# Kernel tuning notes

Hardware: AMD Instinct MI355X
Metric: run time of the kernel (lower is better)

The kernel has to match this reference:

```python
import jax, jax.numpy as jnp
from jax import lax
import numpy as np

B, CIN, COUT, S = 2, 64, 128, 12
H1, H2 = CIN * 4, COUT * 4          # MBConv hidden dims (expand_ratio=4)
HEADS = 8
MLP_HID = COUT * 4                   # transformer mlp_ratio=4
EPS = 1e-5


def conv1x1(x, w, b=None):
    # 1x1x1 Conv3d == channel matmul. w: [out, in], x: [B,C,H,W,D]
    y = jnp.einsum('oc,bchwd->bohwd', w, x)
    if b is not None:
        y = y + b[None, :, None, None, None]
    return y


def inorm(x, g, b):
    # InstanceNorm3d(affine=True): per-sample, per-channel over spatial dims
    m = x.mean(axis=(2, 3, 4), keepdims=True)
    v = x.var(axis=(2, 3, 4), keepdims=True)
    return (x - m) * jax.lax.rsqrt(v + EPS) * g[None, :, None, None, None] + b[None, :, None, None, None]


def gnorm(x, g, b, groups):
    Bb, C, H, W, D = x.shape
    xr = x.reshape(Bb, groups, C // groups, H, W, D)
    m = xr.mean(axis=(2, 3, 4, 5), keepdims=True)
    v = xr.var(axis=(2, 3, 4, 5), keepdims=True)
    xr = (xr - m) * jax.lax.rsqrt(v + EPS)
    return xr.reshape(Bb, C, H, W, D) * g[None, :, None, None, None] + b[None, :, None, None, None]


def dwconv3(x, w):
    # depthwise 3x3x3, stride 1, pad 1. w: [C,1,3,3,3]
    return lax.conv_general_dilated(
        x, w, window_strides=(1, 1, 1), padding=[(1, 1)] * 3,
        dimension_numbers=('NCDHW', 'OIDHW', 'NCDHW'),
        feature_group_count=x.shape[1])


def mbconv(x, ew, g1, b1, dw, g2, b2, sw1, sb1, sw2, sb2, pw, g3, b3, use_residual):
    res = x
    h = jax.nn.silu(inorm(conv1x1(x, ew), g1, b1))        # expand 1x1
    h = jax.nn.silu(inorm(dwconv3(h, dw), g2, b2))        # depthwise 3x3x3
    s = h.mean(axis=(2, 3, 4), keepdims=True)             # SE: squeeze
    s = jax.nn.silu(conv1x1(s, sw1, sb1))
    s = jax.nn.sigmoid(conv1x1(s, sw2, sb2))
    h = h * s
    h = inorm(conv1x1(h, pw), g3, b3)                     # project
    return res + h if use_residual else h


def mhsa(x, qkv_w, proj_w, proj_b):
    Bb, C, H, W, D = x.shape
    N = H * W * D
    hd = C // HEADS
    qkv = conv1x1(x, qkv_w).reshape(Bb, 3, HEADS, hd, N)
    qkv = jnp.transpose(qkv, (1, 0, 2, 4, 3))             # [3,B,h,N,hd]
    q, k, v = qkv[0], qkv[1], qkv[2]
    attn = jax.nn.softmax(jnp.einsum('bhnd,bhmd->bhnm', q, k) * (hd ** -0.5), axis=-1)
    out = jnp.einsum('bhnm,bhmd->bhnd', attn, v)          # [B,h,N,hd]
    out = jnp.transpose(out, (0, 1, 3, 2)).reshape(Bb, C, H, W, D)
    return conv1x1(out, proj_w, proj_b)


def transformer_block(x, n1g, n1b, qkv, pw, pb, n2g, n2b, mw1, mb1, mw2, mb2):
    x = x + mhsa(gnorm(x, n1g, n1b, min(32, x.shape[1])), qkv, pw, pb)
    h = gnorm(x, n2g, n2b, min(32, x.shape[1]))
    h = conv1x1(jax.nn.gelu(conv1x1(h, mw1, mb1), approximate=False), mw2, mb2)
    return x + h


def shuffle_attn(x, cw1, cw2, gng, gnb, sw):
    b, c, h, w, d = x.shape
    G = 4
    gc = c // (2 * G)  # group_channels
    x6 = x.reshape(b, G, 2 * gc, h, w, d)
    x0 = x6[:, :, :gc].reshape(b * G, gc, h, w, d)
    x1 = x6[:, :, gc:].reshape(b * G, gc, h, w, d)
    # channel branch
    a = x0.mean(axis=(2, 3, 4), keepdims=True)
    a = conv1x1(jax.nn.silu(conv1x1(a, cw1)), cw2)
    x0 = jax.nn.sigmoid(a) * x0
    # spatial branch: GroupNorm(max(1,gc//8)=2 groups) + 1x1 conv
    sgn = gnorm(x1, gng, gnb, max(1, gc // 8))
    x1 = jax.nn.sigmoid(conv1x1(sgn, sw)) * x1
    out = jnp.concatenate([x0.reshape(b, G * gc, h, w, d), x1.reshape(b, G * gc, h, w, d)], axis=1)
    # channel shuffle
    out = out.reshape(b, G, 2 * gc, h, w, d).transpose(0, 2, 1, 3, 4, 5).reshape(b, c, h, w, d)
    return out


def setup_inputs() -> dict:
    key = jax.random.key(0)
    ks = iter(jax.random.split(key, 64))
    w = lambda *shape: jax.random.normal(next(ks), shape, jnp.float32) * 0.05
    p = {}
    p['x'] = jax.random.normal(next(ks), (B, CIN, S, S, S), jnp.float32)
    # mbconv1 (in=64 -> hidden=256 -> out=128), SE reduced = 256//4 = 64
    r1 = H1 // 4
    p['m1_ew'] = w(H1, CIN); p['m1_g1'] = jnp.ones(H1); p['m1_b1'] = jnp.zeros(H1)
    p['m1_dw'] = w(H1, 1, 3, 3, 3); p['m1_g2'] = jnp.ones(H1); p['m1_b2'] = jnp.zeros(H1)
    p['m1_sw1'] = w(r1, H1); p['m1_sb1'] = jnp.zeros(r1)
    p['m1_sw2'] = w(H1, r1); p['m1_sb2'] = jnp.zeros(H1)
    p['m1_pw'] = w(COUT, H1); p['m1_g3'] = jnp.ones(COUT); p['m1_b3'] = jnp.zeros(COUT)
    # mbconv2 (in=128 -> hidden=512 -> out=128, residual), SE reduced = 512//4 = 128
    r2 = H2 // 4
    p['m2_ew'] = w(H2, COUT); p['m2_g1'] = jnp.ones(H2); p['m2_b1'] = jnp.zeros(H2)
    p['m2_dw'] = w(H2, 1, 3, 3, 3); p['m2_g2'] = jnp.ones(H2); p['m2_b2'] = jnp.zeros(H2)
    p['m2_sw1'] = w(r2, H2); p['m2_sb1'] = jnp.zeros(r2)
    p['m2_sw2'] = w(H2, r2); p['m2_sb2'] = jnp.zeros(H2)
    p['m2_pw'] = w(COUT, H2); p['m2_g3'] = jnp.ones(COUT); p['m2_b3'] = jnp.zeros(COUT)
    # transformer
    p['t_n1g'] = jnp.ones(COUT); p['t_n1b'] = jnp.zeros(COUT)
    p['t_qkv'] = w(3 * COUT, COUT)
    p['t_pw'] = w(COUT, COUT); p['t_pb'] = jnp.zeros(COUT)
    p['t_n2g'] = jnp.ones(COUT); p['t_n2b'] = jnp.zeros(COUT)
    p['t_mw1'] = w(MLP_HID, COUT); p['t_mb1'] = jnp.zeros(MLP_HID)
    p['t_mw2'] = w(COUT, MLP_HID); p['t_mb2'] = jnp.zeros(COUT)
    # shuffle attention: group_channels = 128 // 8 = 16, channel_fc reduces to 4
    gc = COUT // 8
    p['s_cw1'] = w(max(1, gc // 4), gc); p['s_cw2'] = w(gc, max(1, gc // 4))
    p['s_gng'] = jnp.ones(gc); p['s_gnb'] = jnp.zeros(gc)
    p['s_sw'] = w(gc, gc)
    return p


def reference(x, m1_ew, m1_g1, m1_b1, m1_dw, m1_g2, m1_b2, m1_sw1, m1_sb1, m1_sw2, m1_sb2, m1_pw, m1_g3, m1_b3, m2_ew, m2_g1, m2_b1, m2_dw, m2_g2, m2_b2, m2_sw1, m2_sb1, m2_sw2, m2_sb2, m2_pw, m2_g3, m2_b3, t_n1g, t_n1b, t_qkv, t_pw, t_pb, t_n2g, t_n2b, t_mw1, t_mb1, t_mw2, t_mb2, s_cw1, s_cw2, s_gng, s_gnb, s_sw):
    x = mbconv(x, m1_ew, m1_g1, m1_b1, m1_dw, m1_g2, m1_b2, m1_sw1, m1_sb1, m1_sw2, m1_sb2, m1_pw, m1_g3, m1_b3, use_residual=False)
    x = mbconv(x, m2_ew, m2_g1, m2_b1, m2_dw, m2_g2, m2_b2, m2_sw1, m2_sb1, m2_sw2, m2_sb2, m2_pw, m2_g3, m2_b3, use_residual=True)
    x = transformer_block(x, t_n1g, t_n1b, t_qkv, t_pw, t_pb, t_n2g, t_n2b, t_mw1, t_mb1, t_mw2, t_mb2)
    x = shuffle_attn(x, s_cw1, s_cw2, s_gng, s_gnb, s_sw)
    return x
```

## Files before the change

kernel.cpp:

```cpp
#include <hip/hip_runtime.h>
#include <cmath>

#define NSP 1728
#define BB  2
#define SS  12

typedef __attribute__((ext_vector_type(8))) short short8;
typedef __attribute__((ext_vector_type(4))) short short4v;
typedef __attribute__((ext_vector_type(4))) float floatx4;

__device__ __forceinline__ short f2bf(float f) {
    unsigned u = __float_as_uint(f);
    u += 0x7fff + ((u >> 16) & 1);
    return (short)(u >> 16);
}
__device__ __forceinline__ unsigned pack2bf(float a, float b) {
    unsigned ua = __float_as_uint(a); ua += 0x7fff + ((ua >> 16) & 1);
    unsigned ub = __float_as_uint(b); ub += 0x7fff + ((ub >> 16) & 1);
    return (ua >> 16) | (ub & 0xffff0000u);
}
__device__ __forceinline__ short8 ld8(const short* p) {
    short4v a = *(const short4v*)p;
    short4v b = *(const short4v*)(p + 4);
    return __builtin_shufflevector(a, b, 0, 1, 2, 3, 4, 5, 6, 7);
}
__device__ __forceinline__ float fexp2(float x) {
    float r;
    asm("v_exp_f32 %0, %1" : "=v"(r) : "v"(x));
    return r;
}

__device__ __forceinline__ void block_reduce2(float& s, float& s2) {
    __shared__ float red[8][2];
    __syncthreads();
    #pragma unroll
    for (int o = 32; o; o >>= 1) {
        s  += __shfl_down(s,  o, 64);
        s2 += __shfl_down(s2, o, 64);
    }
    int lane = threadIdx.x & 63, w = threadIdx.x >> 6;
    if (lane == 0) { red[w][0] = s; red[w][1] = s2; }
    __syncthreads();
    int nw = (blockDim.x + 63) >> 6;
    if (threadIdx.x == 0) {
        float a = 0.f, b = 0.f;
        for (int i = 0; i < nw; i++) { a += red[i][0]; b += red[i][1]; }
        red[0][0] = a; red[0][1] = b;
    }
    __syncthreads();
    s = red[0][0]; s2 = red[0][1];
}

#define WTOT 376832
__global__ __launch_bounds__(256) void prep_kernel(
        const float* __restrict__ s0, const float* __restrict__ s1,
        const float* __restrict__ s2, const float* __restrict__ s3,
        const float* __restrict__ s4, const float* __restrict__ s5,
        const float* __restrict__ s6, const float* __restrict__ s7,
        short* __restrict__ dst, float* __restrict__ stz,
        const float* __restrict__ w1a, const float* __restrict__ w2a,
        const float* __restrict__ w1b, const float* __restrict__ w2b,
        float* __restrict__ tsw) {
    if (blockIdx.x < 11) stz[blockIdx.x * 256 + threadIdx.x] = 0.f;
    if (blockIdx.x >= 368) {
        int e = (blockIdx.x - 368) * 1024 + threadIdx.x * 4;
        #pragma unroll
        for (int k = 0; k < 4; k++) {
            int idx = e + k;
            float v;
            if (idx < 16384) {
                int c = idx >> 6, r = idx & 63;
                v = w1a[r * 256 + c];
            } else if (idx < 32768) {
                int l = idx - 16384; int r = l >> 8, ci = l & 255;
                v = w2a[ci * 64 + r];
            } else if (idx < 98304) {
                int l = idx - 32768; int c = l >> 7, r = l & 127;
                v = w1b[r * 512 + c];
            } else {
                int l = idx - 98304; int r = l >> 9, ci = l & 511;
                v = w2b[ci * 128 + r];
            }
            tsw[idx] = v;
        }
        return;
    }
    const int offs[9] = {0, 16384, 49152, 114688, 180224, 229376, 245760, 311296, WTOT};
    const float* srcs[8] = {s0, s1, s2, s3, s4, s5, s6, s7};
    int e = blockIdx.x * 1024 + threadIdx.x * 4;
    #pragma unroll
    for (int k = 0; k < 4; k++) {
        int idx = e + k;
        int seg = 0;
        while (idx >= offs[seg + 1]) seg++;
        dst[idx] = f2bf(srcs[seg][idx - offs[seg]]);
    }
}

template<int CIN, int SER>
__global__ __launch_bounds__(1024) void segate_kernel(
        const float* __restrict__ pooled_in,
        const float* __restrict__ w1t, const float* __restrict__ b1,
        const float* __restrict__ w2t, const float* __restrict__ b2,
        float* __restrict__ gate) {
    __shared__ float pooled[CIN];
    __shared__ float hid[SER];
    __shared__ float part[1024];
    int b = blockIdx.x;
    int tid = threadIdx.x;
    if (tid < CIN) pooled[tid] = pooled_in[b * CIN + tid];
    __syncthreads();
    {
        constexpr int S = 1024 / SER;
        constexpr int CC = CIN / S;
        int r = tid % SER, s = tid / SER;
        const float* wp = w1t + (size_t)(s * CC) * SER + r;
        float a = 0.f;
        #pragma unroll 4
        for (int c = 0; c < CC; c++) a = fmaf(wp[(size_t)c * SER], pooled[s * CC + c], a);
        part[tid] = a;
    }
    __syncthreads();
    if (tid < SER) {
        constexpr int S = 1024 / SER;
        float h = b1[tid];
        #pragma unroll
        for (int s2 = 0; s2 < S; s2++) h += part[s2 * SER + tid];
        hid[tid] = h / (1.f + __expf(-h));
    }
    __syncthreads();
    {
        constexpr int T = 1024 / CIN;
        constexpr int RR = SER / T;
        int ci = tid % CIN, s = tid / CIN;
        const float* wp = w2t + (size_t)(s * RR) * CIN + ci;
        float a = 0.f;
        #pragma unroll 4
        for (int r = 0; r < RR; r++) a = fmaf(wp[(size_t)r * CIN], hid[s * RR + r], a);
        part[tid] = a;
    }
    __syncthreads();
    if (tid < CIN) {
        constexpr int T = 1024 / CIN;
        float g = b2[tid];
        #pragma unroll
        for (int s2 = 0; s2 < T; s2++) g += part[s2 * CIN + tid];
        gate[b * CIN + tid] = 1.f / (1.f + __expf(-g));
    }
}

template<int CIN, int COUT, int COSUB>
__global__ __launch_bounds__(256) void convm_kernel(
        const float* __restrict__ in, const short* __restrict__ inbf,
        const short* __restrict__ wb,
        const float* __restrict__ biasc,
        const float* __restrict__ segate,
        const float* __restrict__ fstats, const float* __restrict__ fg,
        const float* __restrict__ fb, int fgs,
        const float* __restrict__ ing, const float* __restrict__ inb,
        const float* __restrict__ inres,
        float* __restrict__ xout,
        const float* resid, float* out,
        short* __restrict__ obf, int obfm,
        float* stats_out, const float* __restrict__ statres, int act) {
    constexpr int XP = CIN + 8;
    __shared__ float sc[CIN];
    __shared__ float sh[CIN];
    __shared__ float sa[CIN];
    __shared__ float sbl[CIN];
    __shared__ __align__(16) short xa[16 * XP];
    int flat = blockIdx.x;
    int b = flat / 108, mt = flat % 108;
    int n0 = mt * 16;
    int tid = threadIdx.x;

    if (!inbf) {
    if (segate) {
        for (int c = tid; c < CIN; c += 256) {
            sc[c] = segate[b * CIN + c];
            sh[c] = 0.f;
        }
    } else if (ing) {
        for (int c = tid; c < CIN; c += 256) {
            const float* S = fstats + (size_t)(b * CIN + c) * 5;
            float A = S[0], Bq = S[1], Cq = S[2], Dq = S[3], Eq = S[4];
            const float N = (float)NSP;
            float mean = A / N, var = Bq / N - mean * mean;
            float a_ = ing[c] * rsqrtf(var + 1e-5f);
            float b_ = inb[c] - mean * a_;
            sa[c] = a_; sbl[c] = b_;
            sc[c] = a_ * A + b_ * N + Dq;
            sh[c] = a_ * a_ * Bq + 2.f * a_ * b_ * A + b_ * b_ * N
                  + 2.f * a_ * Cq + 2.f * b_ * Dq + Eq;
        }
        __syncthreads();
        float gS = 0.f, gS2 = 0.f;
        if (tid < CIN) {
            int g0 = (tid / fgs) * fgs;
            for (int k = 0; k < fgs; k++) { gS += sc[g0 + k]; gS2 += sh[g0 + k]; }
        }
        __syncthreads();
        if (tid < CIN) {
            float Ng = fgs * (float)NSP;
            float gm = gS / Ng, gv = gS2 / Ng - gm * gm;
            float s_ = rsqrtf(gv + 1e-5f) * fg[tid];
            sc[tid] = s_;
            sh[tid] = fb[tid] - gm * s_;
        }
    } else if (fstats) {
        for (int c = tid; c < CIN; c += 256) {
            int g0 = c / fgs;
            float S = 0.f, S2 = 0.f;
            for (int k = 0; k < fgs; k++) {
                S  += fstats[(b * CIN + g0 * fgs + k) * 2];
                S2 += fstats[(b * CIN + g0 * fgs + k) * 2 + 1];
            }
            float N = fgs * (float)NSP;
            float mean = S / N, var = S2 / N - mean * mean;
            float s = rsqrtf(var + 1e-5f) * fg[c];
            sc[c] = s;
            sh[c] = fb[c] - mean * s;
        }
    } else {
        for (int c = tid; c < CIN; c += 256) { sc[c] = 1.f; sh[c] = 0.f; }
    }
    __syncthreads();

    bool dosw = (xout != nullptr) && (blockIdx.y == 0);
    #pragma unroll
    for (int i = 0; i < CIN / 64; i++) {
        int e = tid + i * 256;
        int ci = e >> 2;
        int jj = (e & 3) * 4;
        size_t gi = ((size_t)b * CIN + ci) * NSP + n0 + jj;
        float4 v4 = *(const float4*)(in + gi);
        float v0, v1, v2, v3;
        if (ing) {
            float4 rr = *(const float4*)(inres + gi);
            float a_ = sa[ci], b_ = sbl[ci];
            float x0 = fmaf(v4.x, a_, b_) + rr.x;
            float x1 = fmaf(v4.y, a_, b_) + rr.y;
            float x2 = fmaf(v4.z, a_, b_) + rr.z;
            float x3 = fmaf(v4.w, a_, b_) + rr.w;
            if (dosw) {
                float4 o; o.x = x0; o.y = x1; o.z = x2; o.w = x3;
                *(float4*)(xout + gi) = o;
            }
            float s_ = sc[ci], h_ = sh[ci];
            v0 = fmaf(x0, s_, h_); v1 = fmaf(x1, s_, h_);
            v2 = fmaf(x2, s_, h_); v3 = fmaf(x3, s_, h_);
        } else {
            float s_ = sc[ci], h_ = sh[ci];
            v0 = fmaf(v4.x, s_, h_); v1 = fmaf(v4.y, s_, h_);
            v2 = fmaf(v4.z, s_, h_); v3 = fmaf(v4.w, s_, h_);
            if (dosw) {
                float4 o; o.x = v0; o.y = v1; o.z = v2; o.w = v3;
                *(float4*)(xout + gi) = o;
            }
        }
        xa[(jj + 0) * XP + ci] = f2bf(v0);
        xa[(jj + 1) * XP + ci] = f2bf(v1);
        xa[(jj + 2) * XP + ci] = f2bf(v2);
        xa[(jj + 3) * XP + ci] = f2bf(v3);
    }
    __syncthreads();
    }

    int lane = tid & 63, wv = tid >> 6;
    int col = lane & 15, quad = lane >> 4;
    short8 afr[CIN / 32];
    if (inbf) {
        const short* ar = inbf + ((size_t)b * 1728 + n0 + col) * CIN;
        #pragma unroll
        for (int kc = 0; kc < CIN / 32; kc++)
            afr[kc] = ld8(ar + kc * 32 + quad * 8);
    } else {
        #pragma unroll
        for (int kc = 0; kc < CIN / 32; kc++)
            afr[kc] = ld8(xa + col * XP + kc * 32 + quad * 8);
    }

    int cobase0 = blockIdx.y * (64 * COSUB) + wv * (16 * COSUB);
    floatx4 acc[COSUB];
    #pragma unroll
    for (int sub = 0; sub < COSUB; sub++) {
        floatx4 a = {0.f, 0.f, 0.f, 0.f};
        const short* wrow = wb + (size_t)(cobase0 + sub * 16 + col) * CIN;
        #pragma unroll
        for (int kc = 0; kc < CIN / 32; kc++) {
            short8 bw = ld8(wrow + kc * 32 + quad * 8);
            a = __builtin_amdgcn_mfma_f32_16x16x32_bf16(afr[kc], bw, a, 0, 0, 0);
        }
        acc[sub] = a;
    }

    #pragma unroll
    for (int sub = 0; sub < COSUB; sub++) {
        int cobase = cobase0 + sub * 16;
        int co = cobase + col;
        float bv = biasc ? biasc[co] : 0.f;
        float r0 = acc[sub][0] + bv, r1 = acc[sub][1] + bv;
        float r2 = acc[sub][2] + bv, r3 = acc[sub][3] + bv;
        if (act == 2) {
            r0 = 0.5f * r0 * (1.f + erff(r0 * 0.70710678118654752f));
            r1 = 0.5f * r1 * (1.f + erff(r1 * 0.70710678118654752f));
            r2 = 0.5f * r2 * (1.f + erff(r2 * 0.70710678118654752f));
            r3 = 0.5f * r3 * (1.f + erff(r3 * 0.70710678118654752f));
        }
        size_t oi = ((size_t)b * COUT + co) * NSP + n0 + quad * 4;
        if (resid) {
            float4 rv = *(const float4*)(resid + oi);
            r0 += rv.x; r1 += rv.y; r2 += rv.z; r3 += rv.w;
        }
        if (obf) {
            if (obfm == 1) {
                if (co < 256) {
                    float s_ = (co < 128) ? 0.36067376022224085f : 1.f;
                    short* qb = obf + (((size_t)(b * 16 + (co >> 4)) * 1728 + n0 + quad * 4) * 16
                                       + (co & 15));
                    qb[0]  = f2bf(r0 * s_);
                    qb[16] = f2bf(r1 * s_);
                    qb[32] = f2bf(r2 * s_);
                    qb[48] = f2bf(r3 * s_);
                } else {
                    short* vb = obf + 884736
                        + ((size_t)(b * 8 + ((co - 256) >> 4)) * 16 + (co & 15)) * 1728
                        + n0 + quad * 4;
                    uint2 pv; pv.x = pack2bf(r0, r1); pv.y = pack2bf(r2, r3);
                    *(uint2*)vb = pv;
                }
            } else {
                short* hb = obf + ((size_t)b * 1728 + n0 + quad * 4) * COUT + co;
                hb[0]        = f2bf(r0);
                hb[COUT]     = f2bf(r1);
                hb[2 * COUT] = f2bf(r2);
                hb[3 * COUT] = f2bf(r3);
            }
        }
        if (out) {
            float4 ov; ov.x = r0; ov.y = r1; ov.z = r2; ov.w = r3;
            *(float4*)(out + oi) = ov;
        }
        if (stats_out) {
            if (statres) {
                float4 rv = *(const float4*)(statres + oi);
                float s   = (r0 + r1) + (r2 + r3);
                float s2  = (r0 * r0 + r1 * r1) + (r2 * r2 + r3 * r3);
                float sx  = (r0 * rv.x + r1 * rv.y) + (r2 * rv.z + r3 * rv.w);
                float sr  = (rv.x + rv.y) + (rv.z + rv.w);
                float sr2 = (rv.x * rv.x + rv.y * rv.y) + (rv.z * rv.z + rv.w * rv.w);
                s   += __shfl_xor(s,   16, 64); s   += __shfl_xor(s,   32, 64);
                s2  += __shfl_xor(s2,  16, 64); s2  += __shfl_xor(s2,  32, 64);
                sx  += __shfl_xor(sx,  16, 64); sx  += __shfl_xor(sx,  32, 64);
                sr  += __shfl_xor(sr,  16, 64); sr  += __shfl_xor(sr,  32, 64);
                sr2 += __shfl_xor(sr2, 16, 64); sr2 += __shfl_xor(sr2, 32, 64);
                if (lane < 16) {
                    float* sp = stats_out + (size_t)(b * COUT + cobase + lane) * 5;
                    atomicAdd(sp + 0, s);
                    atomicAdd(sp + 1, s2);
                    atomicAdd(sp + 2, sx);
                    atomicAdd(sp + 3, sr);
                    atomicAdd(sp + 4, sr2);
                }
            } else {
                float s  = (r0 + r1) + (r2 + r3);
                float s2 = (r0 * r0 + r1 * r1) + (r2 * r2 + r3 * r3);
                s  += __shfl_xor(s,  16, 64);
                s  += __shfl_xor(s,  32, 64);
                s2 += __shfl_xor(s2, 16, 64);
                s2 += __shfl_xor(s2, 32, 64);
                if (lane < 16) {
                    atomicAdd(&stats_out[(b * COUT + cobase + lane) * 2],     s);
                    atomicAdd(&stats_out[(b * COUT + cobase + lane) * 2 + 1], s2);
                }
            }
        }
    }
}

__global__ __launch_bounds__(256) void indw_kernel(
        const float* __restrict__ in,
        const float* __restrict__ g1, const float* __restrict__ b1,
        const float* __restrict__ dw,
        const float* __restrict__ g2, const float* __restrict__ b2,
        float* __restrict__ out, float* __restrict__ se_s, int C) {
    int bc = blockIdx.x;
    int c  = bc % C;
    __shared__ float tile[14 * 14 * 14];
    __shared__ float wsh[27];
    const float* ip = in + (size_t)bc * NSP;
    float r[7];
    float s = 0.f, s2 = 0.f;
    for (int i = threadIdx.x; i < 2744; i += 256) tile[i] = 0.f;
    #pragma unroll
    for (int i = 0; i < 7; i++) {
        int n = threadIdx.x + i * 256;
        if (n < NSP) { r[i] = ip[n]; s += r[i]; s2 += r[i] * r[i]; }
        else r[i] = 0.f;
    }
    if (threadIdx.x < 27) wsh[threadIdx.x] = dw[(size_t)c * 27 + threadIdx.x];
    block_reduce2(s, s2);
    float mean = s / NSP, var = s2 / NSP - (s / NSP) * (s / NSP);
    float rstd = rsqrtf(var + 1e-5f);
    float gc = g1[c], bc1 = b1[c];
    #pragma unroll
    for (int i = 0; i < 7; i++) {
        int n = threadIdx.x + i * 256;
        if (n < NSP) {
            int z = n / 144, y = (n / 12) % 12, x = n % 12;
            float v = (r[i] - mean) * rstd * gc + bc1;
            tile[((z + 1) * 14 + y + 1) * 14 + x + 1] = v / (1.f + __expf(-v));
        }
    }
    __syncthreads();
    float d[7];
    #pragma unroll
    for (int i = 0; i < 7; i++) {
        int n = threadIdx.x + i * 256;
        d[i] = 0.f;
        if (n < NSP) {
            int z = n / 144, y = (n / 12) % 12, x = n % 12;
            const float* ctr = tile + ((z + 1) * 14 + y + 1) * 14 + x + 1;
            float acc = 0.f;
            #pragma unroll
            for (int dz = 0; dz < 3; dz++)
                #pragma unroll
                for (int dy = 0; dy < 3; dy++)
                    #pragma unroll
                    for (int dx = 0; dx < 3; dx++)
                        acc = fmaf(wsh[dz * 9 + dy * 3 + dx],
                                   ctr[(dz - 1) * 196 + (dy - 1) * 14 + (dx - 1)], acc);
            d[i] = acc;
        }
    }
    s = 0.f; s2 = 0.f;
    #pragma unroll
    for (int i = 0; i < 7; i++) {
        int n = threadIdx.x + i * 256;
        if (n < NSP) { s += d[i]; s2 += d[i] * d[i]; }
    }
    block_reduce2(s, s2);
    mean = s / NSP; var = s2 / NSP - mean * mean;
    rstd = rsqrtf(var + 1e-5f);
    float gc2 = g2[c], bc2 = b2[c];
    float ssum = 0.f;
    float* op = out + (size_t)bc * NSP;
    #pragma unroll
    for (int i = 0; i < 7; i++) {
        int n = threadIdx.x + i * 256;
        if (n < NSP) {
            float v = (d[i] - mean) * rstd * gc2 + bc2;
            v = v / (1.f + __expf(-v));
            op[n] = v;
            ssum += v;
        }
    }
    float dummy = 0.f;
    block_reduce2(ssum, dummy);
    if (threadIdx.x == 0) se_s[bc] = ssum / NSP;
}

#define APT 36
__global__ __launch_bounds__(256) void attn_kernel(
        const short* __restrict__ qkbf, const short* __restrict__ vbf,
        float* __restrict__ O) {
    __shared__ __align__(16) short pt[4][16 * APT];
    int bh = blockIdx.x;
    int b = bh >> 3, h = bh & 7;
    int wave = threadIdx.x >> 6, lane = threadIdx.x & 63;
    int m = lane & 15, quad = lane >> 4;
    int q0 = (blockIdx.y * 4 + wave) * 16;
    short* ptw = pt[wave];
    const short* qrow  = qkbf + ((size_t)(b * 16 + h) * 1728 + q0 + m) * 16;
    const short* kbase = qkbf + ((size_t)(b * 16 + 8 + h) * 1728) * 16;
    const short* vbase = vbf + ((size_t)(b * 8 + h) * 16) * 1728;
    short8 qa;
    #pragma unroll
    for (int i = 0; i < 8; i++) qa[i] = 0;
    if (quad < 2) qa = ld8(qrow + quad * 8);
    floatx4 o = {0.f, 0.f, 0.f, 0.f};
    float ls = 0.f;
    #pragma unroll 2
    for (int s = 0; s < 54; s++) {
        int jl = s * 32;
        short8 ak0, ak1;
        #pragma unroll
        for (int i = 0; i < 8; i++) { ak0[i] = 0; ak1[i] = 0; }
        if (quad < 2) {
            ak0 = ld8(kbase + (jl + m) * 16 + quad * 8);
            ak1 = ld8(kbase + (jl + 16 + m) * 16 + quad * 8);
        }
        floatx4 s0 = {0.f, 0.f, 0.f, 0.f}, s1 = {0.f, 0.f, 0.f, 0.f};
        s0 = __builtin_amdgcn_mfma_f32_16x16x32_bf16(ak0, qa, s0, 0, 0, 0);
        s1 = __builtin_amdgcn_mfma_f32_16x16x32_bf16(ak1, qa, s1, 0, 0, 0);
        float p0r0 = fexp2(s0[0]), p0r1 = fexp2(s0[1]), p0r2 = fexp2(s0[2]), p0r3 = fexp2(s0[3]);
        float p1r0 = fexp2(s1[0]), p1r1 = fexp2(s1[1]), p1r2 = fexp2(s1[2]), p1r3 = fexp2(s1[3]);
        ls += (p0r0 + p0r1) + (p0r2 + p0r3) + (p1r0 + p1r1) + (p1r2 + p1r3);
        uint2 w0, w1;
        w0.x = pack2bf(p0r0, p0r1); w0.y = pack2bf(p0r2, p0r3);
        w1.x = pack2bf(p1r0, p1r1); w1.y = pack2bf(p1r2, p1r3);
        *(uint2*)(ptw + m * APT + quad * 4)      = w0;
        *(uint2*)(ptw + m * APT + 16 + quad * 4) = w1;
        short8 av = ld8(vbase + (size_t)m * 1728 + jl + quad * 8);
        short8 pb = ld8(ptw + m * APT + quad * 8);
        o = __builtin_amdgcn_mfma_f32_16x16x32_bf16(av, pb, o, 0, 0, 0);
    }
    ls += __shfl_xor(ls, 16, 64);
    ls += __shfl_xor(ls, 32, 64);
    float inv = 1.f / ls;
    size_t obase = ((size_t)(b * 128 + h * 16 + quad * 4)) * NSP + q0 + m;
    #pragma unroll
    for (int r = 0; r < 4; r++)
        O[obase + (size_t)r * NSP] = o[r] * inv;
}

__global__ void sfinal_kernel(const float* __restrict__ X,
                              const float* __restrict__ st,
                              const float* __restrict__ cw1,
                              const float* __restrict__ cw2,
                              const float* __restrict__ gng,
                              const float* __restrict__ gnb,
                              const float* __restrict__ sw,
                              float* __restrict__ out) {
    int bg = blockIdx.x;
    int b = bg >> 2, g = bg & 3;
    __shared__ float swl[256];
    for (int i = threadIdx.x; i < 256; i += 64) swl[i] = sw[i];
    __syncthreads();
    float pooled[16];
    #pragma unroll
    for (int j = 0; j < 16; j++)
        pooled[j] = st[(b * 128 + g * 32 + j) * 2] * (1.f / NSP);
    float hid[4];
    #pragma unroll
    for (int r = 0; r < 4; r++) {
        float a = 0.f;
        #pragma unroll
        for (int j = 0; j < 16; j++) a = fmaf(cw1[r * 16 + j], pooled[j], a);
        hid[r] = a / (1.f + __expf(-a));
    }
    float gate[16];
    #pragma unroll
    for (int j = 0; j < 16; j++) {
        float a = 0.f;
        #pragma unroll
        for (int r = 0; r < 4; r++) a = fmaf(cw2[j * 4 + r], hid[r], a);
        gate[j] = 1.f / (1.f + __expf(-a));
    }
    float gmean[2], grstd[2];
    #pragma unroll
    for (int t = 0; t < 2; t++) {
        float S = 0.f, S2 = 0.f;
        #pragma unroll
        for (int k = 0; k < 8; k++) {
            int c = g * 32 + 16 + t * 8 + k;
            S  += st[(b * 128 + c) * 2];
            S2 += st[(b * 128 + c) * 2 + 1];
        }
        float N = 8.f * NSP;
        gmean[t] = S / N;
        grstd[t] = rsqrtf(S2 / N - gmean[t] * gmean[t] + 1e-5f);
    }
    int n = blockIdx.y * 64 + threadIdx.x;
    const float* xb = X + (size_t)b * 128 * NSP;
    #pragma unroll
    for (int j = 0; j < 16; j++) {
        float v = xb[(size_t)(g * 32 + j) * NSP + n] * gate[j];
        int k = g * 16 + j;
        int cp = (k % 32) * 4 + (k / 32);
        out[((size_t)b * 128 + cp) * NSP + n] = v;
    }
    float sgn[16];
    #pragma unroll
    for (int j = 0; j < 16; j++) {
        int grp = j >> 3;
        float xv = xb[(size_t)(g * 32 + 16 + j) * NSP + n];
        sgn[j] = (xv - gmean[grp]) * grstd[grp] * gng[j] + gnb[j];
    }
    #pragma unroll
    for (int j = 0; j < 16; j++) {
        float a = 0.f;
        #pragma unroll
        for (int jp = 0; jp < 16; jp++) a = fmaf(swl[j * 16 + jp], sgn[jp], a);
        float v = (1.f / (1.f + __expf(-a))) * xb[(size_t)(g * 32 + 16 + j) * NSP + n];
        int k = 64 + g * 16 + j;
        int cp = (k % 32) * 4 + (k / 32);
        out[((size_t)b * 128 + cp) * NSP + n] = v;
    }
}

extern "C" void kernel_launch(void* const* d_in, const int* in_sizes, int n_in,
                              void* d_out, int out_size, void* d_ws, size_t ws_size,
                              hipStream_t stream) {
    const float* x     = (const float*)d_in[0];
    const float* m1_ew = (const float*)d_in[1];
    const float* m1_g1 = (const float*)d_in[2];
    const float* m1_b1 = (const float*)d_in[3];
    const float* m1_dw = (const float*)d_in[4];
    const float* m1_g2 = (const float*)d_in[5];
    const float* m1_b2 = (const float*)d_in[6];
    const float* m1_sw1= (const float*)d_in[7];
    const float* m1_sb1= (const float*)d_in[8];
    const float* m1_sw2= (const float*)d_in[9];
    const float* m1_sb2= (const float*)d_in[10];
    const float* m1_pw = (const float*)d_in[11];
    const float* m1_g3 = (const float*)d_in[12];
    const float* m1_b3 = (const float*)d_in[13];
    const float* m2_ew = (const float*)d_in[14];
    const float* m2_g1 = (const float*)d_in[15];
    const float* m2_b1 = (const float*)d_in[16];
    const float* m2_dw = (const float*)d_in[17];
    const float* m2_g2 = (const float*)d_in[18];
    const float* m2_b2 = (const float*)d_in[19];
    const float* m2_sw1= (const float*)d_in[20];
    const float* m2_sb1= (const float*)d_in[21];
    const float* m2_sw2= (const float*)d_in[22];
    const float* m2_sb2= (const float*)d_in[23];
    const float* m2_pw = (const float*)d_in[24];
    const float* m2_g3 = (const float*)d_in[25];
    const float* m2_b3 = (const float*)d_in[26];
    const float* t_n1g = (const float*)d_in[27];
    const float* t_n1b = (const float*)d_in[28];
    const float* t_qkv = (const float*)d_in[29];
    const float* t_pw  = (const float*)d_in[30];
    const float* t_pb  = (const float*)d_in[31];
    const float* t_n2g = (const float*)d_in[32];
    const float* t_n2b = (const float*)d_in[33];
    const float* t_mw1 = (const float*)d_in[34];
    const float* t_mb1 = (const float*)d_in[35];
    const float* t_mw2 = (const float*)d_in[36];
    const float* t_mb2 = (const float*)d_in[37];
    const float* s_cw1 = (const float*)d_in[38];
    const float* s_cw2 = (const float*)d_in[39];
    const float* s_gng = (const float*)d_in[40];
    const float* s_gnb = (const float*)d_in[41];
    const float* s_sw  = (const float*)d_in[42];

    float* out = (float*)d_out;

    float* ws = (float*)d_ws;
    float* bufA   = ws;
    float* bufB   = bufA + (size_t)BB * 512 * NSP;
    float* bufX   = bufB + (size_t)BB * 512 * NSP;
    float* bufY   = bufX + (size_t)BB * 128 * NSP;
    float* bufQKV = bufY + (size_t)BB * 128 * NSP;
    float* pl     = bufQKV + (size_t)BB * 384 * NSP;
    float* small  = pl + (size_t)16 * 6 * NSP;
    float* se_s   = small;
    float* st1    = small + 1024;
    float* st3    = small + 1536;
    float* st4    = small + 2048;
    float* st2    = small + 2560;
    float* gate1  = small + 4096;
    float* gate2  = small + 4608;
    short* wbf    = (short*)(small + 8192);
    float* tsw    = small + 196608;
    float* T_M1SW1 = tsw;
    float* T_M1SW2 = tsw + 16384;
    float* T_M2SW1 = tsw + 32768;
    float* T_M2SW2 = tsw + 98304;
    float* bufX2  = tsw + 163840;
    float* bufO   = bufA;
    short* qkbf   = (short*)bufQKV;
    short* hbf    = (short*)bufA;

    short* W_M1EW = wbf + 0;
    short* W_M1PW = wbf + 16384;
    short* W_M2EW = wbf + 49152;
    short* W_M2PW = wbf + 114688;
    short* W_QKV  = wbf + 180224;
    short* W_TPW  = wbf + 229376;
    short* W_MW1  = wbf + 245760;
    short* W_MW2  = wbf + 311296;

    dim3 blk(256);

    prep_kernel<<<528, blk, 0, stream>>>(
        m1_ew, m1_pw, m2_ew, m2_pw, t_qkv, t_pw, t_mw1, t_mw2, wbf, st1,
        m1_sw1, m1_sw2, m2_sw1, m2_sw2, tsw);

    convm_kernel<64, 256, 2><<<dim3(BB * 108, 2), blk, 0, stream>>>(
        x, nullptr, W_M1EW, nullptr, nullptr,
        nullptr, nullptr, nullptr, 0,
        nullptr, nullptr, nullptr,
        nullptr,
        nullptr, bufA, nullptr, 0, nullptr, nullptr, 0);
    indw_kernel<<<BB * 256, blk, 0, stream>>>(bufA, m1_g1, m1_b1, m1_dw, m1_g2, m1_b2, bufB, se_s, 256);
    segate_kernel<256, 64><<<BB, dim3(1024), 0, stream>>>(
        se_s, T_M1SW1, m1_sb1, T_M1SW2, m1_sb2, gate1);
    convm_kernel<256, 128, 1><<<dim3(BB * 108, 2), blk, 0, stream>>>(
        bufB, nullptr, W_M1PW, nullptr, gate1,
        nullptr, nullptr, nullptr, 0,
        nullptr, nullptr, nullptr,
        nullptr,
        nullptr, bufY, nullptr, 0, st1, nullptr, 0);

    convm_kernel<128, 512, 4><<<dim3(BB * 108, 2), blk, 0, stream>>>(
        bufY, nullptr, W_M2EW, nullptr, nullptr,
        st1, m1_g3, m1_b3, 1,
        nullptr, nullptr, nullptr,
        bufX,
        nullptr, bufA, nullptr, 0, nullptr, nullptr, 0);
    indw_kernel<<<BB * 512, blk, 0, stream>>>(bufA, m2_g1, m2_b1, m2_dw, m2_g2, m2_b2, bufB, se_s, 512);
    segate_kernel<512, 128><<<BB, dim3(1024), 0, stream>>>(
        se_s, T_M2SW1, m2_sb1, T_M2SW2, m2_sb2, gate2);
    convm_kernel<512, 128, 1><<<dim3(BB * 108, 2), blk, 0, stream>>>(
        bufB, nullptr, W_M2PW, nullptr, gate2,
        nullptr, nullptr, nullptr, 0,
        nullptr, nullptr, nullptr,
        nullptr,
        nullptr, bufY, nullptr, 0, st2, bufX, 0);

    convm_kernel<128, 384, 3><<<dim3(BB * 108, 2), blk, 0, stream>>>(
        bufY, nullptr, W_QKV, nullptr, nullptr,
        st2, t_n1g, t_n1b, 4,
        m2_g3, m2_b3, bufX,
        bufX2,
        nullptr, nullptr, qkbf, 1, nullptr, nullptr, 0);
    attn_kernel<<<dim3(16, 27), blk, 0, stream>>>(qkbf, qkbf + 884736, bufO);
    convm_kernel<128, 128, 1><<<dim3(BB * 108, 2), blk, 0, stream>>>(
        bufO, nullptr, W_TPW, t_pb, nullptr,
        nullptr, nullptr, nullptr, 0,
        nullptr, nullptr, nullptr,
        nullptr,
        bufX2, bufX2, nullptr, 0, st3, nullptr, 0);
    convm_kernel<128, 512, 4><<<dim3(BB * 108, 2), blk, 0, stream>>>(
        bufX2, nullptr, W_MW1, t_mb1, nullptr,
        st3, t_n2g, t_n2b, 4,
        nullptr, nullptr, nullptr,
        nullptr,
        nullptr, nullptr, hbf, 2, nullptr, nullptr, 2);
    convm_kernel<512, 128, 1><<<dim3(BB * 108, 2), blk, 0, stream>>>(
        nullptr, hbf, W_MW2, t_mb2, nullptr,
        nullptr, nullptr, nullptr, 0,
        nullptr, nullptr, nullptr,
        nullptr,
        bufX2, bufX2, nullptr, 0, st4, nullptr, 0);

    sfinal_kernel<<<dim3(BB * 4, 27), dim3(64), 0, stream>>>(
        bufX2, st4, s_cw1, s_cw2, s_gng, s_gnb, s_sw, out);
}
```

Baseline: 319.4 us.

## Split 1x1 conv and attention into single-wave blocks, one 16-channel tile each

The 1x1 conv kernel now uses 64-thread blocks, each computing one 16x16 output tile, with the output-channel groups spread across a much larger grid.y instead of 4 waves each doing several sub-tiles. The attention kernel likewise drops to one wave per block with four times as many blocks. The goal is more parallel blocks and better GPU fill for this small problem. The cost is that every block now redoes the per-channel norm setup and the input staging/bf16 conversion for its tile, so input reads and prologue work grow in proportion to the number of channel groups.

```diff
diff --git a/kernel.cpp b/kernel.cpp
--- a/kernel.cpp
+++ b/kernel.cpp
@@ -149,8 +149,8 @@
     }
 }
 
-template<int CIN, int COUT, int COSUB>
-__global__ __launch_bounds__(256) void convm_kernel(
+template<int CIN, int COUT, bool DIRECT>
+__global__ __launch_bounds__(64) void convw_kernel(
         const float* __restrict__ in, const short* __restrict__ inbf,
         const short* __restrict__ wb,
         const float* __restrict__ biasc,
@@ -164,24 +164,26 @@
         short* __restrict__ obf, int obfm,
         float* stats_out, const float* __restrict__ statres, int act) {
     constexpr int XP = CIN + 8;
-    __shared__ float sc[CIN];
-    __shared__ float sh[CIN];
-    __shared__ float sa[CIN];
-    __shared__ float sbl[CIN];
-    __shared__ __align__(16) short xa[16 * XP];
+    __shared__ float sc[DIRECT ? 1 : CIN];
+    __shared__ float sh[DIRECT ? 1 : CIN];
+    __shared__ float sa[(!DIRECT && CIN <= 128) ? CIN : 1];
+    __shared__ float sbl[(!DIRECT && CIN <= 128) ? CIN : 1];
+    __shared__ __align__(16) short xa[DIRECT ? 8 : 16 * XP];
     int flat = blockIdx.x;
     int b = flat / 108, mt = flat % 108;
     int n0 = mt * 16;
     int tid = threadIdx.x;
-
-    if (!inbf) {
+    int cg = blockIdx.y;
+
+    if constexpr (!DIRECT) {
     if (segate) {
-        for (int c = tid; c < CIN; c += 256) {
+        for (int c = tid; c < CIN; c += 64) {
             sc[c] = segate[b * CIN + c];
             sh[c] = 0.f;
         }
-    } else if (ing) {
-        for (int c = tid; c < CIN; c += 256) {
+    } else if (CIN <= 128 && ing) {
+        constexpr int NC = (CIN + 63) / 64;
+        for (int c = tid; c < CIN; c += 64) {
             const float* S = fstats + (size_t)(b * CIN + c) * 5;
             float A = S[0], Bq = S[1], Cq = S[2], Dq = S[3], Eq = S[4];
             const float N = (float)NSP;
@@ -194,21 +196,29 @@
                   + 2.f * a_ * Cq + 2.f * b_ * Dq + Eq;
         }
         __syncthreads();
-        float gS = 0.f, gS2 = 0.f;
-        if (tid < CIN) {
-            int g0 = (tid / fgs) * fgs;
-            for (int k = 0; k < fgs; k++) { gS += sc[g0 + k]; gS2 += sh[g0 + k]; }
+        float tS[NC], tH[NC];
+        {
+            int k2 = 0;
+            for (int c = tid; c < CIN; c += 64, k2++) {
+                int g0 = (c / fgs) * fgs;
+                float gS = 0.f, gS2 = 0.f;
+                for (int k = 0; k < fgs; k++) { gS += sc[g0 + k]; gS2 += sh[g0 + k]; }
+                tS[k2] = gS; tH[k2] = gS2;
+            }
         }
         __syncthreads();
-        if (tid < CIN) {
-            float Ng = fgs * (float)NSP;
-            float gm = gS / Ng, gv = gS2 / Ng - gm * gm;
-            float s_ = rsqrtf(gv + 1e-5f) * fg[tid];
-            sc[tid] = s_;
-            sh[tid] = fb[tid] - gm * s_;
+        {
+            int k2 = 0;
+            for (int c = tid; c < CIN; c += 64, k2++) {
+                float Ng = fgs * (float)NSP;
+                float gm = tS[k2] / Ng, gv = tH[k2] / Ng - gm * gm;
+                float s_ = rsqrtf(gv + 1e-5f) * fg[c];
+                sc[c] = s_;
+                sh[c] = fb[c] - gm * s_;
+            }
         }
     } else if (fstats) {
-        for (int c = tid; c < CIN; c += 256) {
+        for (int c = tid; c < CIN; c += 64) {
             int g0 = c / fgs;
             float S = 0.f, S2 = 0.f;
             for (int k = 0; k < fgs; k++) {
@@ -222,20 +232,20 @@
             sh[c] = fb[c] - mean * s;
         }
     } else {
-        for (int c = tid; c < CIN; c += 256) { sc[c] = 1.f; sh[c] = 0.f; }
-    }
-    __syncthreads();
-
-    bool dosw = (xout != nullptr) && (blockIdx.y == 0);
-    #pragma unroll
-    for (int i = 0; i < CIN / 64; i++) {
-        int e = tid + i * 256;
+        for (int c = tid; c < CIN; c += 64) { sc[c] = 1.f; sh[c] = 0.f; }
+    }
+    __syncthreads();
+
+    bool dosw = (xout != nullptr) && (cg == 0);
+    #pragma unroll
+    for (int i = 0; i < CIN / 16; i++) {
+        int e = tid + i * 64;
         int ci = e >> 2;
         int jj = (e & 3) * 4;
         size_t gi = ((size_t)b * CIN + ci) * NSP + n0 + jj;
         float4 v4 = *(const float4*)(in + gi);
         float v0, v1, v2, v3;
-        if (ing) {
+        if (CIN <= 128 && ing) {
             float4 rr = *(const float4*)(inres + gi);
             float a_ = sa[ci], b_ = sbl[ci];
             float x0 = fmaf(v4.x, a_, b_) + rr.x;
@@ -266,10 +276,9 @@
     __syncthreads();
     }
 
-    int lane = tid & 63, wv = tid >> 6;
-    int col = lane & 15, quad = lane >> 4;
+    int col = tid & 15, quad = tid >> 4;
     short8 afr[CIN / 32];
-    if (inbf) {
+    if constexpr (DIRECT) {
         const short* ar = inbf + ((size_t)b * 1728 + n0 + col) * CIN;
         #pragma unroll
         for (int kc = 0; kc < CIN / 32; kc++)
@@ -280,99 +289,88 @@
             afr[kc] = ld8(xa + col * XP + kc * 32 + quad * 8);
     }
 
-    int cobase0 = blockIdx.y * (64 * COSUB) + wv * (16 * COSUB);
-    floatx4 acc[COSUB];
-    #pragma unroll
-    for (int sub = 0; sub < COSUB; sub++) {
-        floatx4 a = {0.f, 0.f, 0.f, 0.f};
-        const short* wrow = wb + (size_t)(cobase0 + sub * 16 + col) * CIN;
-        #pragma unroll
-        for (int kc = 0; kc < CIN / 32; kc++) {
-            short8 bw = ld8(wrow + kc * 32 + quad * 8);
-            a = __builtin_amdgcn_mfma_f32_16x16x32_bf16(afr[kc], bw, a, 0, 0, 0);
-        }
-        acc[sub] = a;
-    }
-
-    #pragma unroll
-    for (int sub = 0; sub < COSUB; sub++) {
-        int cobase = cobase0 + sub * 16;
-        int co = cobase + col;
-        float bv = biasc ? biasc[co] : 0.f;
-        float r0 = acc[sub][0] + bv, r1 = acc[sub][1] + bv;
-        float r2 = acc[sub][2] + bv, r3 = acc[sub][3] + bv;
-        if (act == 2) {
-            r0 = 0.5f * r0 * (1.f + erff(r0 * 0.70710678118654752f));
-            r1 = 0.5f * r1 * (1.f + erff(r1 * 0.70710678118654752f));
-            r2 = 0.5f * r2 * (1.f + erff(r2 * 0.70710678118654752f));
-            r3 = 0.5f * r3 * (1.f + erff(r3 * 0.70710678118654752f));
-        }
-        size_t oi = ((size_t)b * COUT + co) * NSP + n0 + quad * 4;
-        if (resid) {
-            float4 rv = *(const float4*)(resid + oi);
-            r0 += rv.x; r1 += rv.y; r2 += rv.z; r3 += rv.w;
-        }
-        if (obf) {
-            if (obfm == 1) {
-                if (co < 256) {
-                    float s_ = (co < 128) ? 0.36067376022224085f : 1.f;
-                    short* qb = obf + (((size_t)(b * 16 + (co >> 4)) * 1728 + n0 + quad * 4) * 16
-                                       + (co & 15));
-                    qb[0]  = f2bf(r0 * s_);
-                    qb[16] = f2bf(r1 * s_);
-                    qb[32] = f2bf(r2 * s_);
-                    qb[48] = f2bf(r3 * s_);
-                } else {
-                    short* vb = obf + 884736
-                        + ((size_t)(b * 8 + ((co - 256) >> 4)) * 16 + (co & 15)) * 1728
-                        + n0 + quad * 4;
-                    uint2 pv; pv.x = pack2bf(r0, r1); pv.y = pack2bf(r2, r3);
-                    *(uint2*)vb = pv;
-                }
+    int cobase = cg * 16;
+    int co = cobase + col;
+    const short* wrow = wb + (size_t)co * CIN;
+    floatx4 acc = {0.f, 0.f, 0.f, 0.f};
+    #pragma unroll
+    for (int kc = 0; kc < CIN / 32; kc++) {
+        short8 bw = ld8(wrow + kc * 32 + quad * 8);
+        acc = __builtin_amdgcn_mfma_f32_16x16x32_bf16(afr[kc], bw, acc, 0, 0, 0);
+    }
+    float bv = biasc ? biasc[co] : 0.f;
+    float r0 = acc[0] + bv, r1 = acc[1] + bv, r2 = acc[2] + bv, r3 = acc[3] + bv;
+    if (act == 2) {
+        r0 = 0.5f * r0 * (1.f + erff(r0 * 0.70710678118654752f));
+        r1 = 0.5f * r1 * (1.f + erff(r1 * 0.70710678118654752f));
+        r2 = 0.5f * r2 * (1.f + erff(r2 * 0.70710678118654752f));
+        r3 = 0.5f * r3 * (1.f + erff(r3 * 0.70710678118654752f));
+    }
+    size_t oi = ((size_t)b * COUT + co) * NSP + n0 + quad * 4;
+    if (resid) {
+        float4 rv = *(const float4*)(resid + oi);
+        r0 += rv.x; r1 += rv.y; r2 += rv.z; r3 += rv.w;
+    }
+    if (obf) {
+        if (obfm == 1) {
+            if (co < 256) {
+                float s_ = (co < 128) ? 0.36067376022224085f : 1.f;
+                short* qb = obf + (((size_t)(b * 16 + (co >> 4)) * 1728 + n0 + quad * 4) * 16
+                                   + (co & 15));
+                qb[0]  = f2bf(r0 * s_);
+                qb[16] = f2bf(r1 * s_);
+                qb[32] = f2bf(r2 * s_);
+                qb[48] = f2bf(r3 * s_);
             } else {
-                short* hb = obf + ((size_t)b * 1728 + n0 + quad * 4) * COUT + co;
-                hb[0]        = f2bf(r0);
-                hb[COUT]     = f2bf(r1);
-                hb[2 * COUT] = f2bf(r2);
-                hb[3 * COUT] = f2bf(r3);
-            }
-        }
-        if (out) {
-            float4 ov; ov.x = r0; ov.y = r1; ov.z = r2; ov.w = r3;
-            *(float4*)(out + oi) = ov;
-        }
-        if (stats_out) {
-            if (statres) {
-                float4 rv = *(const float4*)(statres + oi);
-                float s   = (r0 + r1) + (r2 + r3);
-                float s2  = (r0 * r0 + r1 * r1) + (r2 * r2 + r3 * r3);
-                float sx  = (r0 * rv.x + r1 * rv.y) + (r2 * rv.z + r3 * rv.w);
-                float sr  = (rv.x + rv.y) + (rv.z + rv.w);
-                float sr2 = (rv.x * rv.x + rv.y * rv.y) + (rv.z * rv.z + rv.w * rv.w);
-                s   += __shfl_xor(s,   16, 64); s   += __shfl_xor(s,   32, 64);
-                s2  += __shfl_xor(s2,  16, 64); s2  += __shfl_xor(s2,  32, 64);
-                sx  += __shfl_xor(sx,  16, 64); sx  += __shfl_xor(sx,  32, 64);
-                sr  += __shfl_xor(sr,  16, 64); sr  += __shfl_xor(sr,  32, 64);
-                sr2 += __shfl_xor(sr2, 16, 64); sr2 += __shfl_xor(sr2, 32, 64);
-                if (lane < 16) {
-                    float* sp = stats_out + (size_t)(b * COUT + cobase + lane) * 5;
-                    atomicAdd(sp + 0, s);
-                    atomicAdd(sp + 1, s2);
-                    atomicAdd(sp + 2, sx);
-                    atomicAdd(sp + 3, sr);
-                    atomicAdd(sp + 4, sr2);
-                }
-            } else {
-                float s  = (r0 + r1) + (r2 + r3);
-                float s2 = (r0 * r0 + r1 * r1) + (r2 * r2 + r3 * r3);
-                s  += __shfl_xor(s,  16, 64);
-                s  += __shfl_xor(s,  32, 64);
-                s2 += __shfl_xor(s2, 16, 64);
-                s2 += __shfl_xor(s2, 32, 64);
-                if (lane < 16) {
-                    atomicAdd(&stats_out[(b * COUT + cobase + lane) * 2],     s);
-                    atomicAdd(&stats_out[(b * COUT + cobase + lane) * 2 + 1], s2);
-                }
+                short* vb = obf + 884736
+                    + ((size_t)(b * 8 + ((co - 256) >> 4)) * 16 + (co & 15)) * 1728
+                    + n0 + quad * 4;
+                uint2 pv; pv.x = pack2bf(r0, r1); pv.y = pack2bf(r2, r3);
+                *(uint2*)vb = pv;
+            }
+        } else {
+            short* hb = obf + ((size_t)b * 1728 + n0 + quad * 4) * COUT + co;
+            hb[0]        = f2bf(r0);
+            hb[COUT]     = f2bf(r1);
+            hb[2 * COUT] = f2bf(r2);
+            hb[3 * COUT] = f2bf(r3);
+        }
+    }
+    if (out) {
+        float4 ov; ov.x = r0; ov.y = r1; ov.z = r2; ov.w = r3;
+        *(float4*)(out + oi) = ov;
+    }
+    if (stats_out) {
+        if (statres) {
+            float4 rv = *(const float4*)(statres + oi);
+            float s   = (r0 + r1) + (r2 + r3);
+            float s2  = (r0 * r0 + r1 * r1) + (r2 * r2 + r3 * r3);
+            float sx  = (r0 * rv.x + r1 * rv.y) + (r2 * rv.z + r3 * rv.w);
+            float sr  = (rv.x + rv.y) + (rv.z + rv.w);
+            float sr2 = (rv.x * rv.x + rv.y * rv.y) + (rv.z * rv.z + rv.w * rv.w);
+            s   += __shfl_xor(s,   16, 64); s   += __shfl_xor(s,   32, 64);
+            s2  += __shfl_xor(s2,  16, 64); s2  += __shfl_xor(s2,  32, 64);
+            sx  += __shfl_xor(sx,  16, 64); sx  += __shfl_xor(sx,  32, 64);
+            sr  += __shfl_xor(sr,  16, 64); sr  += __shfl_xor(sr,  32, 64);
+            sr2 += __shfl_xor(sr2, 16, 64); sr2 += __shfl_xor(sr2, 32, 64);
+            if (tid < 16) {
+                float* sp = stats_out + (size_t)(b * COUT + cobase + tid) * 5;
+                atomicAdd(sp + 0, s);
+                atomicAdd(sp + 1, s2);
+                atomicAdd(sp + 2, sx);
+                atomicAdd(sp + 3, sr);
+                atomicAdd(sp + 4, sr2);
+            }
+        } else {
+            float s  = (r0 + r1) + (r2 + r3);
+            float s2 = (r0 * r0 + r1 * r1) + (r2 * r2 + r3 * r3);
+            s  += __shfl_xor(s,  16, 64);
+            s  += __shfl_xor(s,  32, 64);
+            s2 += __shfl_xor(s2, 16, 64);
+            s2 += __shfl_xor(s2, 32, 64);
+            if (tid < 16) {
+                atomicAdd(&stats_out[(b * COUT + cobase + tid) * 2],     s);
+                atomicAdd(&stats_out[(b * COUT + cobase + tid) * 2 + 1], s2);
             }
         }
     }
@@ -461,16 +459,15 @@
 }
 
 #define APT 36
-__global__ __launch_bounds__(256) void attn_kernel(
+__global__ __launch_bounds__(64) void attn_kernel(
         const short* __restrict__ qkbf, const short* __restrict__ vbf,
         float* __restrict__ O) {
-    __shared__ __align__(16) short pt[4][16 * APT];
+    __shared__ __align__(16) short pt[16 * APT];
     int bh = blockIdx.x;
     int b = bh >> 3, h = bh & 7;
-    int wave = threadIdx.x >> 6, lane = threadIdx.x & 63;
+    int lane = threadIdx.x;
     int m = lane & 15, quad = lane >> 4;
-    int q0 = (blockIdx.y * 4 + wave) * 16;
-    short* ptw = pt[wave];
+    int q0 = blockIdx.y * 16;
     const short* qrow  = qkbf + ((size_t)(b * 16 + h) * 1728 + q0 + m) * 16;
     const short* kbase = qkbf + ((size_t)(b * 16 + 8 + h) * 1728) * 16;
     const short* vbase = vbf + ((size_t)(b * 8 + h) * 16) * 1728;
@@ -499,10 +496,10 @@
         uint2 w0, w1;
         w0.x = pack2bf(p0r0, p0r1); w0.y = pack2bf(p0r2, p0r3);
         w1.x = pack2bf(p1r0, p1r1); w1.y = pack2bf(p1r2, p1r3);
-        *(uint2*)(ptw + m * APT + quad * 4)      = w0;
-        *(uint2*)(ptw + m * APT + 16 + quad * 4) = w1;
+        *(uint2*)(pt + m * APT + quad * 4)      = w0;
+        *(uint2*)(pt + m * APT + 16 + quad * 4) = w1;
         short8 av = ld8(vbase + (size_t)m * 1728 + jl + quad * 8);
-        short8 pb = ld8(ptw + m * APT + quad * 8);
+        short8 pb = ld8(pt + m * APT + quad * 8);
         o = __builtin_amdgcn_mfma_f32_16x16x32_bf16(av, pb, o, 0, 0, 0);
     }
     ls += __shfl_xor(ls, 16, 64);
@@ -674,12 +671,13 @@
     short* W_MW2  = wbf + 311296;
 
     dim3 blk(256);
+    dim3 wblk(64);
 
     prep_kernel<<<528, blk, 0, stream>>>(
         m1_ew, m1_pw, m2_ew, m2_pw, t_qkv, t_pw, t_mw1, t_mw2, wbf, st1,
         m1_sw1, m1_sw2, m2_sw1, m2_sw2, tsw);
 
-    convm_kernel<64, 256, 2><<<dim3(BB * 108, 2), blk, 0, stream>>>(
+    convw_kernel<64, 256, false><<<dim3(BB * 108, 16), wblk, 0, stream>>>(
         x, nullptr, W_M1EW, nullptr, nullptr,
         nullptr, nullptr, nullptr, 0,
         nullptr, nullptr, nullptr,
@@ -688,14 +686,14 @@
     indw_kernel<<<BB * 256, blk, 0, stream>>>(bufA, m1_g1, m1_b1, m1_dw, m1_g2, m1_b2, bufB, se_s, 256);
     segate_kernel<256, 64><<<BB, dim3(1024), 0, stream>>>(
         se_s, T_M1SW1, m1_sb1, T_M1SW2, m1_sb2, gate1);
-    convm_kernel<256, 128, 1><<<dim3(BB * 108, 2), blk, 0, stream>>>(
+    convw_kernel<256, 128, false><<<dim3(BB * 108, 8), wblk, 0, stream>>>(
         bufB, nullptr, W_M1PW, nullptr, gate1,
         nullptr, nullptr, nullptr, 0,
         nullptr, nullptr, nullptr,
         nullptr,
         nullptr, bufY, nullptr, 0, st1, nullptr, 0);
 
-    convm_kernel<128, 512, 4><<<dim3(BB * 108, 2), blk, 0, stream>>>(
+    convw_kernel<128, 512, false><<<dim3(BB * 108, 32), wblk, 0, stream>>>(
         bufY, nullptr, W_M2EW, nullptr, nullptr,
         st1, m1_g3, m1_b3, 1,
         nullptr, nullptr, nullptr,
@@ -704,33 +702,33 @@
     indw_kernel<<<BB * 512, blk, 0, stream>>>(bufA, m2_g1, m2_b1, m2_dw, m2_g2, m2_b2, bufB, se_s, 512);
     segate_kernel<512, 128><<<BB, dim3(1024), 0, stream>>>(
         se_s, T_M2SW1, m2_sb1, T_M2SW2, m2_sb2, gate2);
-    convm_kernel<512, 128, 1><<<dim3(BB * 108, 2), blk, 0, stream>>>(
+    convw_kernel<512, 128, false><<<dim3(BB * 108, 8), wblk, 0, stream>>>(
         bufB, nullptr, W_M2PW, nullptr, gate2,
         nullptr, nullptr, nullptr, 0,
         nullptr, nullptr, nullptr,
         nullptr,
         nullptr, bufY, nullptr, 0, st2, bufX, 0);
 
-    convm_kernel<128, 384, 3><<<dim3(BB * 108, 2), blk, 0, stream>>>(
+    convw_kernel<128, 384, false><<<dim3(BB * 108, 24), wblk, 0, stream>>>(
         bufY, nullptr, W_QKV, nullptr, nullptr,
         st2, t_n1g, t_n1b, 4,
         m2_g3, m2_b3, bufX,
         bufX2,
         nullptr, nullptr, qkbf, 1, nullptr, nullptr, 0);
-    attn_kernel<<<dim3(16, 27), blk, 0, stream>>>(qkbf, qkbf + 884736, bufO);
-    convm_kernel<128, 128, 1><<<dim3(BB * 108, 2), blk, 0, stream>>>(
+    attn_kernel<<<dim3(16, 108), wblk, 0, stream>>>(qkbf, qkbf + 884736, bufO);
+    convw_kernel<128, 128, false><<<dim3(BB * 108, 8), wblk, 0, stream>>>(
         bufO, nullptr, W_TPW, t_pb, nullptr,
         nullptr, nullptr, nullptr, 0,
         nullptr, nullptr, nullptr,
         nullptr,
         bufX2, bufX2, nullptr, 0, st3, nullptr, 0);
-    convm_kernel<128, 512, 4><<<dim3(BB * 108, 2), blk, 0, stream>>>(
+    convw_kernel<128, 512, false><<<dim3(BB * 108, 32), wblk, 0, stream>>>(
         bufX2, nullptr, W_MW1, t_mb1, nullptr,
         st3, t_n2g, t_n2b, 4,
         nullptr, nullptr, nullptr,
         nullptr,
         nullptr, nullptr, hbf, 2, nullptr, nullptr, 2);
-    convm_kernel<512, 128, 1><<<dim3(BB * 108, 2), blk, 0, stream>>>(
+    convw_kernel<512, 128, true><<<dim3(BB * 108, 8), wblk, 0, stream>>>(
         nullptr, hbf, W_MW2, t_mb2, nullptr,
         nullptr, nullptr, nullptr, 0,
         nullptr, nullptr, nullptr,
```

New measurement: 339.9 us. 1.06x slower.
